# Kernel optimization log

Measured on AMD Instinct MI355X. Metric: run time of the kernel, lower is better.

The kernel has to match this reference:

```python
import jax, jax.numpy as jnp
import numpy as np

B, T, DM, DFE, DH, DRH = 32, 2048, 128, 64, 64, 64
E, NF, NSF, TOPK = 8, 16, 64, 2
LN_EPS = 1e-5


def setup_inputs() -> dict:
    key = jax.random.key(0)
    ks = jax.random.split(key, 18)
    s = 0.05
    # base expert i owns columns [16*i, 16*i+16); scale=2 -> expert e uses base e//2
    expert_idx = jnp.asarray(np.stack([np.arange(NF) + NF * (e // 2) for e in range(E)]), dtype=jnp.int32)  # [E,NF]
    stage_idx = jnp.arange(NSF, dtype=jnp.int32)  # stage uses all 64 columns
    return {
        'hidden': jax.random.normal(ks[0], (B, T, DM), jnp.float32),
        'feat': jax.random.normal(ks[1], (B, T, NSF), jnp.float32),
        'ln_g': jnp.ones((DM,), jnp.float32),
        'ln_b': jnp.zeros((DM,), jnp.float32),
        'Wp': jax.random.normal(ks[2], (NSF, DFE), jnp.float32) * s,
        'bp': jnp.zeros((DFE,), jnp.float32),
        'Wr1': jax.random.normal(ks[3], (DM + DFE, DRH), jnp.float32) * s,
        'br1': jnp.zeros((DRH,), jnp.float32),
        'Wr2': jax.random.normal(ks[4], (DRH, E), jnp.float32) * s,
        'br2': jnp.zeros((E,), jnp.float32),
        'Wf': jax.random.normal(ks[5], (E, NF, DFE), jnp.float32) * s,
        'bf': jnp.zeros((E, DFE), jnp.float32),
        'We1h': jax.random.normal(ks[6], (E, DM, DH), jnp.float32) * s,
        'We1f': jax.random.normal(ks[7], (E, DFE, DH), jnp.float32) * s,
        'be1': jnp.zeros((E, DH), jnp.float32),
        'We2': jax.random.normal(ks[8], (E, DH, DM), jnp.float32) * s,
        'be2': jnp.zeros((E, DM), jnp.float32),
        'alpha': jnp.asarray(1.0, jnp.float32),
        'item_seq_len': jax.random.randint(ks[9], (B,), 1, T + 1),
        'expert_idx': expert_idx,
        'stage_idx': stage_idx,
    }


def _layernorm(x, g, b):
    mu = jnp.mean(x, -1, keepdims=True)
    v = jnp.mean(jnp.square(x - mu), -1, keepdims=True)
    return (x - mu) * jax.lax.rsqrt(v + LN_EPS) * g + b


def reference(hidden, feat, ln_g, ln_b, Wp, bp, Wr1, br1, Wr2, br2,
              Wf, bf, We1h, We1f, be1, We2, be2, alpha,
              item_seq_len, expert_idx, stage_idx):
    h = _layernorm(hidden, ln_g, ln_b)                         # [B,T,DM]  pre_ln
    femb = feat[..., stage_idx] @ Wp + bp                      # [B,T,DFE] stage feature projection
    # --- token router: MLP -> softmax(temp=1) -> top-k renormalized gates ---
    rin = jnp.concatenate([h, femb], -1)                       # [B,T,DM+DFE]
    logits = jax.nn.relu(rin @ Wr1 + br1) @ Wr2 + br2          # [B,T,E]
    probs = jax.nn.softmax(logits, axis=-1)
    topv, topi = jax.lax.top_k(probs, TOPK)                    # [B,T,K]
    topv = topv / jnp.sum(topv, -1, keepdims=True)
    gates = jnp.sum(jax.nn.one_hot(topi, E, dtype=probs.dtype) * topv[..., None], axis=-2)  # [B,T,E]
    valid = jnp.arange(T)[None, :] < item_seq_len[:, None]     # [B,T]
    gates = gates * valid[..., None].astype(gates.dtype)
    # --- experts: per-expert feature gather + 2-layer GELU MLP (hidden + feat inputs) ---
    ef = feat[:, :, expert_idx]                                # [B,T,E,NF] gather
    x = jnp.einsum('btef,efd->bted', ef, Wf) + bf              # [B,T,E,DFE]
    h1 = jax.nn.gelu(jnp.einsum('btd,edo->bteo', h, We1h)
                     + jnp.einsum('bted,edo->bteo', x, We1f) + be1, approximate=False)
    eo = jnp.einsum('bteo,eod->bted', h1, We2) + be2           # [B,T,E,DM]
    moe = jnp.einsum('bte,bted->btd', gates, eo)               # weighted combine
    next_hidden = hidden + alpha * moe                         # residual, alpha_scale=1, dropout=0
    return next_hidden, gates, probs
```

## Files before the change

kernel.cpp:

```cpp
#include <hip/hip_runtime.h>
#include <hip/hip_bf16.h>


typedef unsigned short u16;
typedef __attribute__((ext_vector_type(8))) short bfrag;
typedef __attribute__((ext_vector_type(8))) u16 u16x8;
typedef __attribute__((ext_vector_type(4))) float facc;
typedef __attribute__((ext_vector_type(4))) float f32x4;

#define NTOK 65536
#define CAP 65536

#define OFF_CNT   ((size_t)0)
#define OFF_LTOK  ((size_t)512)
#define OFF_SMAPG (OFF_LTOK + (size_t)8*CAP*4)
#define OFF_HWS   (OFF_SMAPG + (size_t)NTOK*8)
#define OFF_EOTOK (OFF_HWS + (size_t)NTOK*128*2)
#define OFF_W1T   (OFF_EOTOK + (size_t)NTOK*2*128*2)
#define OFF_W2T   (OFF_W1T + 163840)
#define OFF_B1P   (OFF_W2T + 131072)
#define OFF_WPR   (OFF_B1P + 2048)
#define OFF_BR1P  (OFF_WPR + 16384)

__device__ __forceinline__ u16 f2bf(float f) {
  union { __hip_bfloat16 h; u16 u; } cv;
  cv.h = __float2bfloat16(f);
  return cv.u;
}
__device__ __forceinline__ float bf2f(u16 u) {
  return __uint_as_float(((unsigned)u) << 16);
}

__global__ __launch_bounds__(256)
void k0_pre(const float* __restrict__ Wp, const float* __restrict__ bp,
            const float* __restrict__ Wr1, const float* __restrict__ br1,
            const float* __restrict__ Wf, const float* __restrict__ bfv,
            const float* __restrict__ We1h, const float* __restrict__ We1f,
            const float* __restrict__ be1, const float* __restrict__ We2,
            float* __restrict__ Wpr, float* __restrict__ br1p,
            u16* __restrict__ w1t, u16* __restrict__ w2t, float* __restrict__ b1p)
{
  int j = blockIdx.x * 256 + threadIdx.x;
  if (j < 4096) {
    int i = j >> 6, o = j & 63;
    float s = 0.f;
    for (int k = 0; k < 64; ++k) s += Wp[i*64+k] * Wr1[(128+k)*64 + o];
    Wpr[i*64+o] = s;
  } else if (j < 4160) {
    int o = j - 4096;
    float s = br1[o];
    for (int k = 0; k < 64; ++k) s += bp[k] * Wr1[(128+k)*64 + o];
    br1p[o] = s;
  } else if (j < 4160 + 81920) {
    int idx = j - 4160;
    int e = idx / 10240; int rem = idx % 10240;
    int jj = rem / 160; int k = rem % 160;
    float v = 0.f;
    if (k < 128) v = We1h[(e*128 + k)*64 + jj];
    else if (k < 144) {
      int i = k - 128; float s = 0.f;
      for (int d = 0; d < 64; ++d) s += Wf[(e*16+i)*64 + d] * We1f[(e*64+d)*64 + jj];
      v = s;
    }
    w1t[(size_t)(e*64 + jj)*160 + k] = f2bf(v);
  } else if (j < 4160 + 81920 + 65536) {
    int idx = j - 4160 - 81920;
    int e = idx / 8192; int rem = idx % 8192;
    int d = rem / 64; int k = rem & 63;
    w2t[(size_t)(e*128 + d)*64 + k] = f2bf(We2[(e*64 + k)*128 + d]);
  } else if (j < 4160 + 81920 + 65536 + 512) {
    int idx = j - 4160 - 81920 - 65536;
    int e = idx >> 6, o = idx & 63;
    float s = be1[e*64 + o];
    for (int d = 0; d < 64; ++d) s += bfv[e*64 + d] * We1f[(e*64+d)*64 + o];
    b1p[e*64 + o] = s;
  }
}

__global__ __launch_bounds__(256, 4)
void k1_router(const float* __restrict__ hidden, const float* __restrict__ feat,
               const float* __restrict__ ln_g, const float* __restrict__ ln_b,
               const float* __restrict__ Wr1, const float* __restrict__ Wr2,
               const float* __restrict__ br2, const int* __restrict__ seqlen,
               const int* __restrict__ sidx_g,
               const float* __restrict__ Wpr, const float* __restrict__ br1p,
               float* __restrict__ outG, float* __restrict__ outP,
               u16* __restrict__ hws, int* __restrict__ cnt,
               int* __restrict__ listTok, float* __restrict__ smapG)
{
  __shared__ float At[64*64];
  __shared__ float Wc[64*64];
  __shared__ float sW2[512];
  __shared__ float sb1[64], sg[128], sb[128], sbr2[8];
  __shared__ int ssidx[64];
  __shared__ int lcnt[8], lbase[8];
  __shared__ int ltok[8][64];
  __shared__ float tg[64][2];

  int tid = threadIdx.x;

  f32x4 wpf[4];
  #pragma unroll
  for (int u = 0; u < 4; ++u) wpf[u] = ((const f32x4*)Wr1)[u*256 + tid];

  for (int i = tid; i < 512; i += 256) sW2[i] = Wr2[i];
  if (tid < 128) sg[tid] = ln_g[tid]; else sb[tid-128] = ln_b[tid-128];
  if (tid < 64) { sb1[tid] = br1p[tid]; ssidx[tid] = sidx_g[tid]; }
  if (tid >= 64 && tid < 72) sbr2[tid-64] = br2[tid-64];
  if (tid >= 72 && tid < 80) lcnt[tid-72] = 0;
  __syncthreads();

  int tok = tid >> 2, q = tid & 3;
  int t = blockIdx.x * 64 + tok;

  f32x4 x[8];
  #pragma unroll
  for (int i = 0; i < 8; ++i) x[i] = *(const f32x4*)(hidden + (size_t)t*128 + q*32 + i*4);
  float s = 0.f;
  #pragma unroll
  for (int i = 0; i < 8; ++i) { s += x[i][0] + x[i][1]; s += x[i][2] + x[i][3]; }
  s += __shfl_xor(s, 1, 64); s += __shfl_xor(s, 2, 64);
  float mu = s * (1.f/128.f);
  float v = 0.f;
  #pragma unroll
  for (int i = 0; i < 8; ++i) {
    #pragma unroll
    for (int j = 0; j < 4; ++j) { float d = x[i][j] - mu; v = fmaf(d, d, v); }
  }
  v += __shfl_xor(v, 1, 64); v += __shfl_xor(v, 2, 64);
  float rs = rsqrtf(v * (1.f/128.f) + 1e-5f);
  #pragma unroll
  for (int i = 0; i < 8; ++i) {
    #pragma unroll
    for (int j = 0; j < 4; ++j) {
      int c = q*32 + i*4 + j;
      x[i][j] = (x[i][j] - mu) * rs * sg[c] + sb[c];
    }
  }
  #pragma unroll
  for (int m = 0; m < 4; ++m) {
    u16x8 o;
    #pragma unroll
    for (int j = 0; j < 4; ++j) { o[j] = f2bf(x[2*m][j]); o[4+j] = f2bf(x[2*m+1][j]); }
    *(u16x8*)(hws + (size_t)t*128 + q*32 + m*8) = o;
  }
  float fv[16];
  #pragma unroll
  for (int i = 0; i < 16; ++i) fv[i] = feat[(size_t)t*64 + ssidx[q*16 + i]];

  float acc[4][4];
  #pragma unroll
  for (int i = 0; i < 4; ++i)
    #pragma unroll
    for (int p = 0; p < 4; ++p) acc[i][p] = 0.f;

  int tb = tid >> 4;
  int ob = (tid & 15) * 4;

  #pragma unroll 1
  for (int c = 0; c < 3; ++c) {
    if (c < 2) {
      if ((c == 0) ? (q < 2) : (q >= 2)) {
        int kbase = (c == 0) ? q*32 : (q-2)*32;
        #pragma unroll
        for (int i = 0; i < 8; ++i)
          #pragma unroll
          for (int j = 0; j < 4; ++j) {
            int kr = kbase + i*4 + j;
            int slot = ((tok >> 2) ^ (kr & 15) ^ (kr >> 4)) & 15;
            *(float*)((char*)At + (kr << 8) + (slot << 4) + ((tok & 3) << 2)) = x[i][j];
          }
      }
    } else {
      #pragma unroll
      for (int i = 0; i < 16; ++i) {
        int kr = q*16 + i;
        int slot = ((tok >> 2) ^ (kr & 15) ^ (kr >> 4)) & 15;
        *(float*)((char*)At + (kr << 8) + (slot << 4) + ((tok & 3) << 2)) = fv[i];
      }
    }
    #pragma unroll
    for (int u = 0; u < 4; ++u) ((f32x4*)Wc)[u*256 + tid] = wpf[u];
    __syncthreads();
    if (c < 2) {
      const f32x4* nsrc = (c == 0) ? (const f32x4*)(Wr1 + 4096) : (const f32x4*)Wpr;
      #pragma unroll
      for (int u = 0; u < 4; ++u) wpf[u] = nsrc[u*256 + tid];
    }
    #pragma unroll 4
    for (int k = 0; k < 64; ++k) {
      int slot = (tb ^ (k & 15) ^ (k >> 4)) & 15;
      f32x4 a4 = *(const f32x4*)((const char*)At + (k << 8) + (slot << 4));
      f32x4 b4 = *(const f32x4*)(Wc + k*64 + ob);
      #pragma unroll
      for (int i = 0; i < 4; ++i)
        #pragma unroll
        for (int p = 0; p < 4; ++p)
          acc[i][p] = fmaf(a4[i], b4[p], acc[i][p]);
    }
    __syncthreads();
  }

  float w2r[4][8];
  #pragma unroll
  for (int p = 0; p < 4; ++p)
    #pragma unroll
    for (int e = 0; e < 8; ++e) w2r[p][e] = sW2[(ob + p)*8 + e];
  float b1r[4];
  #pragma unroll
  for (int p = 0; p < 4; ++p) b1r[p] = sb1[ob + p];

  int j16 = tid & 15;
  #pragma unroll 1
  for (int ti = 0; ti < 4; ++ti) {
    float lo[8];
    #pragma unroll
    for (int e = 0; e < 8; ++e) lo[e] = 0.f;
    #pragma unroll
    for (int p = 0; p < 4; ++p) {
      float z = fmaxf(acc[ti][p] + b1r[p], 0.f);
      #pragma unroll
      for (int e = 0; e < 8; ++e) lo[e] = fmaf(z, w2r[p][e], lo[e]);
    }
    #pragma unroll
    for (int m = 1; m < 16; m <<= 1) {
      #pragma unroll
      for (int e = 0; e < 8; ++e) lo[e] += __shfl_xor(lo[e], m, 64);
    }
    #pragma unroll
    for (int e = 0; e < 8; ++e) lo[e] += sbr2[e];

    int tloc = tb*4 + ti;
    int tt = blockIdx.x*64 + tloc;
    float mx = lo[0];
    #pragma unroll
    for (int e = 1; e < 8; ++e) mx = fmaxf(mx, lo[e]);
    float ex[8]; float ss = 0.f;
    #pragma unroll
    for (int e = 0; e < 8; ++e) { ex[e] = __expf(lo[e] - mx); ss += ex[e]; }
    float inv = 1.f / ss;
    float p[8];
    #pragma unroll
    for (int e = 0; e < 8; ++e) p[e] = ex[e] * inv;
    float p1 = p[0]; int i1 = 0;
    #pragma unroll
    for (int e = 1; e < 8; ++e) { bool tk2 = p[e] > p1; p1 = tk2 ? p[e] : p1; i1 = tk2 ? e : i1; }
    float p2 = -1.f; int i2 = 0;
    #pragma unroll
    for (int e = 0; e < 8; ++e) { bool tk2 = (e != i1) && (p[e] > p2); p2 = tk2 ? p[e] : p2; i2 = tk2 ? e : i2; }
    bool valid = (tt & 2047) < seqlen[tt >> 11];
    float gden = 1.f / (p1 + p2);
    float g1 = p1 * gden, g2 = p2 * gden;
    float pv = p[0];
    #pragma unroll
    for (int e = 1; e < 8; ++e) pv = (j16 == e) ? p[e] : pv;
    if (j16 < 8) outP[(size_t)tt*8 + j16] = pv;
    float gv = (j16 == i1) ? g1 : ((j16 == i2) ? g2 : 0.f);
    if (!valid) gv = 0.f;
    if (j16 < 8) outG[(size_t)tt*8 + j16] = gv;
    if (j16 == 0) {
      if (valid) {
        int lp = atomicAdd(&lcnt[i1], 1); ltok[i1][lp] = (tt << 1);
        lp = atomicAdd(&lcnt[i2], 1);     ltok[i2][lp] = (tt << 1) | 1;
        tg[tloc][0] = g1; tg[tloc][1] = g2;
      } else {
        tg[tloc][0] = 0.f; tg[tloc][1] = 0.f;
      }
    }
  }

  __syncthreads();
  if (tid < 8) lbase[tid] = atomicAdd(&cnt[tid], lcnt[tid]);
  __syncthreads();
  #pragma unroll 1
  for (int e = 0; e < 8; ++e) {
    int ncnt = lcnt[e];
    if (tid < ncnt) listTok[(size_t)e*CAP + lbase[e] + tid] = ltok[e][tid];
  }
  if (tid < 64) {
    float2 g; g.x = tg[tid][0]; g.y = tg[tid][1];
    ((float2*)smapG)[blockIdx.x*64 + tid] = g;
  }
}

__global__ __launch_bounds__(256)
void k2_experts(const float* __restrict__ feat, const u16* __restrict__ hws,
                const u16* __restrict__ w1t, const u16* __restrict__ w2t,
                const float* __restrict__ b1p, const float* __restrict__ be2,
                const int* __restrict__ eidx_g, const int* __restrict__ cnt,
                const int* __restrict__ listTok, u16* __restrict__ eoTok)
{
  __shared__ u16 Xs[64*168];
  __shared__ u16 H1s[64*88];
  __shared__ float b1s[64], be2s[128];
  __shared__ int sent[64];
  __shared__ int seidx[16];
  __shared__ int snr;

  int b = blockIdx.x, tid = threadIdx.x;
  int e = -1, row0 = 0, n = 0, accb = 0;
  #pragma unroll
  for (int i = 0; i < 8; ++i) {
    int ci = cnt[i]; int ns = (ci + 63) >> 6;
    if (e < 0 && b < accb + ns) { e = i; row0 = (b - accb) << 6; n = ci; }
    accb += ns;
  }
  if (e < 0) return;
  int nr = n - row0; if (nr > 64) nr = 64;
  if (tid == 0) snr = nr;

  if (tid < 64) {
    int ent = (tid < nr) ? listTok[(size_t)e*CAP + row0 + tid] : 0;
    sent[tid] = ent;
    b1s[tid] = b1p[e*64 + tid];
  } else if (tid < 192) {
    be2s[tid - 64] = be2[e*128 + tid - 64];
  } else if (tid < 208) {
    seidx[tid-192] = eidx_g[e*16 + tid - 192];
  }
  __syncthreads();

  for (int c2 = tid; c2 < 1024; c2 += 256) {
    int r = c2 >> 4, p = c2 & 15;
    u16x8 vv = *(const u16x8*)(hws + (size_t)(sent[r] >> 1)*128 + p*8);
    *(u16x8*)((char*)Xs + r*336 + p*16) = vv;
  }
  if (tid < 128) {
    int r = tid >> 1, hf = tid & 1;
    int tk = sent[r] >> 1;
    u16x8 ov;
    #pragma unroll
    for (int p = 0; p < 8; ++p) ov[p] = f2bf(feat[(size_t)tk*64 + seidx[hf*8 + p]]);
    *(u16x8*)((char*)Xs + r*336 + 256 + hf*16) = ov;
    u16x8 zv = {0,0,0,0,0,0,0,0};
    *(u16x8*)((char*)Xs + r*336 + 288 + hf*16) = zv;
  }
  __syncthreads();

  int w = tid >> 6, lane = tid & 63;
  int la = lane & 15, lg = lane >> 4;
  const u16* w1e = w1t + (size_t)e*64*160;
  const u16* w2e = w2t + (size_t)e*128*64;

  facc acc[4];
  #pragma unroll
  for (int ni = 0; ni < 4; ++ni) { facc z = {0.f,0.f,0.f,0.f}; acc[ni] = z; }
  #pragma unroll
  for (int kc = 0; kc < 5; ++kc) {
    int r = w*16 + la;
    bfrag af = *(const bfrag*)((const char*)Xs + r*336 + kc*64 + lg*16);
    #pragma unroll
    for (int ni = 0; ni < 4; ++ni) {
      bfrag bf2 = *(const bfrag*)(w1e + (size_t)(ni*16 + la)*160 + kc*32 + lg*8);
      acc[ni] = __builtin_amdgcn_mfma_f32_16x16x32_bf16(af, bf2, acc[ni], 0, 0, 0);
    }
  }
  #pragma unroll
  for (int ni = 0; ni < 4; ++ni)
    #pragma unroll
    for (int rg = 0; rg < 4; ++rg) {
      int r = w*16 + lg*4 + rg;
      int c = ni*16 + la;
      float z = acc[ni][rg] + b1s[c];
      float gl = 0.5f * z * (1.f + erff(z * 0.70710678118f));
      *(u16*)((char*)H1s + r*176 + c*2) = f2bf(gl);
    }
  __syncthreads();

  facc acc2[8];
  #pragma unroll
  for (int ni = 0; ni < 8; ++ni) { facc z = {0.f,0.f,0.f,0.f}; acc2[ni] = z; }
  #pragma unroll
  for (int kc = 0; kc < 2; ++kc) {
    int r = w*16 + la;
    bfrag af = *(const bfrag*)((const char*)H1s + r*176 + kc*64 + lg*16);
    #pragma unroll
    for (int ni = 0; ni < 8; ++ni) {
      bfrag bf2 = *(const bfrag*)(w2e + (size_t)(ni*16 + la)*64 + kc*32 + lg*8);
      acc2[ni] = __builtin_amdgcn_mfma_f32_16x16x32_bf16(af, bf2, acc2[ni], 0, 0, 0);
    }
  }
  #pragma unroll
  for (int ni = 0; ni < 8; ++ni)
    #pragma unroll
    for (int rg = 0; rg < 4; ++rg) {
      int r = w*16 + lg*4 + rg;
      int c = ni*16 + la;
      if (r < snr) {
        float vv = acc2[ni][rg] + be2s[c];
        eoTok[(size_t)sent[r]*128 + c] = f2bf(vv);
      }
    }
}

__global__ __launch_bounds__(256)
void k3_combine(const float* __restrict__ hidden, const float* __restrict__ smapG,
                const u16* __restrict__ eoTok, const float* __restrict__ alphap,
                float* __restrict__ outN)
{
  int tid = threadIdx.x;
  int tok = tid >> 2, q = tid & 3;
  int t = blockIdx.x*64 + tok;
  float2 g = ((const float2*)smapG)[t];
  float a = alphap[0];
  float ag0 = a * g.x, ag1 = a * g.y;
  const f32x4* hp = (const f32x4*)(hidden + (size_t)t*128 + q*32);
  f32x4* op = (f32x4*)(outN + (size_t)t*128 + q*32);
  const u16x8* e0 = (const u16x8*)(eoTok + ((size_t)t*2)*128 + q*32);
  const u16x8* e1 = (const u16x8*)(eoTok + ((size_t)t*2 + 1)*128 + q*32);
  #pragma unroll
  for (int i = 0; i < 4; ++i) {
    f32x4 r0 = hp[2*i], r1 = hp[2*i+1];
    if (g.x != 0.f) {
      u16x8 x0 = e0[i];
      #pragma unroll
      for (int j = 0; j < 4; ++j) { r0[j] = fmaf(ag0, bf2f(x0[j]), r0[j]); r1[j] = fmaf(ag0, bf2f(x0[4+j]), r1[j]); }
    }
    if (g.y != 0.f) {
      u16x8 x1 = e1[i];
      #pragma unroll
      for (int j = 0; j < 4; ++j) { r0[j] = fmaf(ag1, bf2f(x1[j]), r0[j]); r1[j] = fmaf(ag1, bf2f(x1[4+j]), r1[j]); }
    }
    op[2*i] = r0; op[2*i+1] = r1;
  }
}

extern "C" void kernel_launch(void* const* d_in, const int* in_sizes, int n_in,
                              void* d_out, int out_size, void* d_ws, size_t ws_size,
                              hipStream_t stream) {
  const float* hidden = (const float*)d_in[0];
  const float* feat   = (const float*)d_in[1];
  const float* ln_g   = (const float*)d_in[2];
  const float* ln_b   = (const float*)d_in[3];
  const float* Wp     = (const float*)d_in[4];
  const float* bp     = (const float*)d_in[5];
  const float* Wr1    = (const float*)d_in[6];
  const float* br1    = (const float*)d_in[7];
  const float* Wr2    = (const float*)d_in[8];
  const float* br2    = (const float*)d_in[9];
  const float* Wf     = (const float*)d_in[10];
  const float* bfv    = (const float*)d_in[11];
  const float* We1h   = (const float*)d_in[12];
  const float* We1f   = (const float*)d_in[13];
  const float* be1    = (const float*)d_in[14];
  const float* We2    = (const float*)d_in[15];
  const float* be2    = (const float*)d_in[16];
  const float* alpha  = (const float*)d_in[17];
  const int* seqlen   = (const int*)d_in[18];
  const int* eidx     = (const int*)d_in[19];
  const int* sidx     = (const int*)d_in[20];

  char* ws = (char*)d_ws;
  int*   cnt      = (int*)(ws + OFF_CNT);
  int*   listTok  = (int*)(ws + OFF_LTOK);
  float* smapG    = (float*)(ws + OFF_SMAPG);
  u16*   hws      = (u16*)(ws + OFF_HWS);
  u16*   eoTok    = (u16*)(ws + OFF_EOTOK);
  u16*   w1t      = (u16*)(ws + OFF_W1T);
  u16*   w2t      = (u16*)(ws + OFF_W2T);
  float* b1p      = (float*)(ws + OFF_B1P);
  float* Wpr      = (float*)(ws + OFF_WPR);
  float* br1p     = (float*)(ws + OFF_BR1P);

  float* outN = (float*)d_out;
  float* outG = outN + (size_t)NTOK * 128;
  float* outP = outG + (size_t)NTOK * 8;

  hipMemsetAsync(ws + OFF_CNT, 0, 256, stream);
  k0_pre<<<595, 256, 0, stream>>>(Wp, bp, Wr1, br1, Wf, bfv, We1h, We1f, be1, We2,
                                  Wpr, br1p, w1t, w2t, b1p);
  k1_router<<<1024, 256, 0, stream>>>(hidden, feat, ln_g, ln_b, Wr1, Wr2, br2, seqlen,
                                      sidx, Wpr, br1p, outG, outP, hws, cnt,
                                      listTok, smapG);
  k2_experts<<<2056, 256, 0, stream>>>(feat, hws, w1t, w2t, b1p, be2, eidx,
                                       cnt, listTok, eoTok);
  k3_combine<<<1024, 256, 0, stream>>>(hidden, smapG, eoTok, alpha, outN);
}
```

Baseline: 131.6 us.

## Restructure preprocessing, double router tokens per block, add contiguous-index fast paths

The weight-preprocessing kernel now runs as 25 blocks that stage weights in shared memory and do small tiled matmuls, replacing 595 blocks of scalar dot products. It also writes flags recording whether the stage and expert index arrays are contiguous. The router handles 128 tokens per block with 2 threads per token, which halves its grid, reuses each weight tile over twice as many tokens, and aliases shared buffers. When the flags show contiguous indices, the feature gathers in the router and expert kernels use vectorized loads, and the router per-block lists are capped at 128 entries.

```diff
diff --git a/kernel.cpp b/kernel.cpp
--- a/kernel.cpp
+++ b/kernel.cpp
@@ -12,6 +12,7 @@
 #define CAP 65536
 
 #define OFF_CNT   ((size_t)0)
+#define OFF_FLG   ((size_t)64)
 #define OFF_LTOK  ((size_t)512)
 #define OFF_SMAPG (OFF_LTOK + (size_t)8*CAP*4)
 #define OFF_HWS   (OFF_SMAPG + (size_t)NTOK*8)
@@ -32,187 +33,272 @@
 }
 
 __global__ __launch_bounds__(256)
-void k0_pre(const float* __restrict__ Wp, const float* __restrict__ bp,
-            const float* __restrict__ Wr1, const float* __restrict__ br1,
-            const float* __restrict__ Wf, const float* __restrict__ bfv,
-            const float* __restrict__ We1h, const float* __restrict__ We1f,
-            const float* __restrict__ be1, const float* __restrict__ We2,
-            float* __restrict__ Wpr, float* __restrict__ br1p,
-            u16* __restrict__ w1t, u16* __restrict__ w2t, float* __restrict__ b1p)
+void k0a_pre(const float* __restrict__ Wp, const float* __restrict__ bp,
+             const float* __restrict__ Wr1, const float* __restrict__ br1,
+             const float* __restrict__ Wf, const float* __restrict__ bfv,
+             const float* __restrict__ We1h, const float* __restrict__ We1f,
+             const float* __restrict__ be1, const float* __restrict__ We2,
+             const int* __restrict__ eidx_g, const int* __restrict__ sidx_g,
+             float* __restrict__ Wpr, float* __restrict__ br1p,
+             u16* __restrict__ w1t, u16* __restrict__ w2t, float* __restrict__ b1p,
+             int* __restrict__ flags)
 {
-  int j = blockIdx.x * 256 + threadIdx.x;
-  if (j < 4096) {
-    int i = j >> 6, o = j & 63;
-    float s = 0.f;
-    for (int k = 0; k < 64; ++k) s += Wp[i*64+k] * Wr1[(128+k)*64 + o];
-    Wpr[i*64+o] = s;
-  } else if (j < 4160) {
-    int o = j - 4096;
-    float s = br1[o];
-    for (int k = 0; k < 64; ++k) s += bp[k] * Wr1[(128+k)*64 + o];
-    br1p[o] = s;
-  } else if (j < 4160 + 81920) {
-    int idx = j - 4160;
-    int e = idx / 10240; int rem = idx % 10240;
-    int jj = rem / 160; int k = rem % 160;
-    float v = 0.f;
-    if (k < 128) v = We1h[(e*128 + k)*64 + jj];
-    else if (k < 144) {
-      int i = k - 128; float s = 0.f;
-      for (int d = 0; d < 64; ++d) s += Wf[(e*16+i)*64 + d] * We1f[(e*64+d)*64 + jj];
-      v = s;
-    }
-    w1t[(size_t)(e*64 + jj)*160 + k] = f2bf(v);
-  } else if (j < 4160 + 81920 + 65536) {
-    int idx = j - 4160 - 81920;
-    int e = idx / 8192; int rem = idx % 8192;
-    int d = rem / 64; int k = rem & 63;
-    w2t[(size_t)(e*128 + d)*64 + k] = f2bf(We2[(e*64 + k)*128 + d]);
-  } else if (j < 4160 + 81920 + 65536 + 512) {
-    int idx = j - 4160 - 81920 - 65536;
-    int e = idx >> 6, o = idx & 63;
-    float s = be1[e*64 + o];
-    for (int d = 0; d < 64; ++d) s += bfv[e*64 + d] * We1f[(e*64+d)*64 + o];
-    b1p[e*64 + o] = s;
-  }
-}
-
-__global__ __launch_bounds__(256, 4)
+  __shared__ float smA[64*68];
+  __shared__ float smB[128*68];
+  int b = blockIdx.x, tid = threadIdx.x;
+
+  if (b == 0) {
+    for (int idx = tid; idx < 4096; idx += 256) {
+      int r = idx >> 6, c = idx & 63;
+      smA[r*68 + c] = Wp[idx];
+      smB[r*68 + c] = Wr1[128*64 + idx];
+    }
+    if (tid == 0) { int ok = 1; for (int i = 0; i < 64; ++i) ok &= (sidx_g[i] == i); flags[0] = ok; }
+    __syncthreads();
+    int i = tid >> 2, oq = (tid & 3) * 16;
+    f32x4 acc[4];
+    #pragma unroll
+    for (int m = 0; m < 4; ++m) { f32x4 z = {0,0,0,0}; acc[m] = z; }
+    for (int k = 0; k < 64; ++k) {
+      float a = smA[i*68 + k];
+      #pragma unroll
+      for (int m = 0; m < 4; ++m) {
+        f32x4 b4 = *(const f32x4*)(smB + k*68 + oq + m*4);
+        #pragma unroll
+        for (int j = 0; j < 4; ++j) acc[m][j] = fmaf(a, b4[j], acc[m][j]);
+      }
+    }
+    #pragma unroll
+    for (int m = 0; m < 4; ++m) *(f32x4*)(Wpr + i*64 + oq + m*4) = acc[m];
+    if (tid < 64) {
+      float s = br1[tid];
+      for (int k = 0; k < 64; ++k) s = fmaf(bp[k], smB[k*68 + tid], s);
+      br1p[tid] = s;
+    }
+  } else if (b <= 8) {
+    int e = b - 1;
+    for (int idx = tid; idx < 4096; idx += 256) {
+      int r = idx >> 6, c = idx & 63;
+      smB[r*68 + c] = We1f[e*4096 + idx];
+    }
+    for (int idx = tid; idx < 1024; idx += 256) {
+      int r = idx >> 6, c = idx & 63;
+      smA[r*68 + c] = Wf[e*1024 + idx];
+    }
+    if (tid == 0) {
+      int s0 = eidx_g[e*16]; int ok = 1;
+      for (int i = 0; i < 16; ++i) ok &= (eidx_g[e*16 + i] == s0 + i);
+      flags[1 + e] = ok ? s0 : -1;
+    }
+    __syncthreads();
+    int i = tid >> 4, jq = (tid & 15) * 4;
+    f32x4 acc = {0,0,0,0};
+    for (int d = 0; d < 64; ++d) {
+      float a = smA[i*68 + d];
+      f32x4 b4 = *(const f32x4*)(smB + d*68 + jq);
+      #pragma unroll
+      for (int j = 0; j < 4; ++j) acc[j] = fmaf(a, b4[j], acc[j]);
+    }
+    #pragma unroll
+    for (int j = 0; j < 4; ++j) w1t[(size_t)(e*64 + jq + j)*160 + 128 + i] = f2bf(acc[j]);
+    if (tid < 64) {
+      float s = be1[e*64 + tid];
+      for (int d = 0; d < 64; ++d) s = fmaf(bfv[e*64 + d], smB[d*68 + tid], s);
+      b1p[e*64 + tid] = s;
+    }
+    for (int idx = tid; idx < 1024; idx += 256) {
+      int jj = idx >> 4, kk = idx & 15;
+      w1t[(size_t)(e*64 + jj)*160 + 144 + kk] = 0;
+    }
+  } else if (b <= 16) {
+    int e = b - 9;
+    for (int idx = tid; idx < 8192; idx += 256) {
+      int r = idx >> 6, c = idx & 63;
+      smB[r*68 + c] = We1h[(size_t)e*8192 + idx];
+    }
+    __syncthreads();
+    int jj = tid & 63, kb = (tid >> 6) * 32;
+    #pragma unroll
+    for (int m = 0; m < 4; ++m) {
+      u16x8 o;
+      #pragma unroll
+      for (int q = 0; q < 8; ++q) o[q] = f2bf(smB[(kb + m*8 + q)*68 + jj]);
+      *(u16x8*)(w1t + (size_t)(e*64 + jj)*160 + kb + m*8) = o;
+    }
+  } else if (b <= 24) {
+    int e = b - 17;
+    for (int idx = tid; idx < 8192; idx += 256) {
+      int r = idx >> 7, c = idx & 127;
+      smB[r*132 + c] = We2[(size_t)e*8192 + idx];
+    }
+    __syncthreads();
+    int d = tid & 127, kb = (tid >> 7) * 32;
+    #pragma unroll
+    for (int m = 0; m < 4; ++m) {
+      u16x8 o;
+      #pragma unroll
+      for (int q = 0; q < 8; ++q) o[q] = f2bf(smB[(kb + m*8 + q)*132 + d]);
+      *(u16x8*)(w2t + (size_t)(e*128 + d)*64 + kb + m*8) = o;
+    }
+  }
+}
+
+__global__ __launch_bounds__(256, 3)
 void k1_router(const float* __restrict__ hidden, const float* __restrict__ feat,
                const float* __restrict__ ln_g, const float* __restrict__ ln_b,
                const float* __restrict__ Wr1, const float* __restrict__ Wr2,
                const float* __restrict__ br2, const int* __restrict__ seqlen,
                const int* __restrict__ sidx_g,
                const float* __restrict__ Wpr, const float* __restrict__ br1p,
+               const int* __restrict__ flags,
                float* __restrict__ outG, float* __restrict__ outP,
                u16* __restrict__ hws, int* __restrict__ cnt,
                int* __restrict__ listTok, float* __restrict__ smapG)
 {
-  __shared__ float At[64*64];
+  __shared__ __align__(16) char smemAt[64*128*4];
   __shared__ float Wc[64*64];
-  __shared__ float sW2[512];
-  __shared__ float sb1[64], sg[128], sb[128], sbr2[8];
+  __shared__ float sg[128], sb[128], sb1[64], sbr2[8];
   __shared__ int ssidx[64];
   __shared__ int lcnt[8], lbase[8];
-  __shared__ int ltok[8][64];
-  __shared__ float tg[64][2];
+  float* At = (float*)smemAt;
+  int* ltok = (int*)smemAt;
+  float* tgp = (float*)(smemAt + 4096);
 
   int tid = threadIdx.x;
 
   f32x4 wpf[4];
   #pragma unroll
-  for (int u = 0; u < 4; ++u) wpf[u] = ((const f32x4*)Wr1)[u*256 + tid];
-
-  for (int i = tid; i < 512; i += 256) sW2[i] = Wr2[i];
+  for (int u = 0; u < 4; ++u) wpf[u] = ((const f32x4*)Wpr)[u*256 + tid];
+
   if (tid < 128) sg[tid] = ln_g[tid]; else sb[tid-128] = ln_b[tid-128];
   if (tid < 64) { sb1[tid] = br1p[tid]; ssidx[tid] = sidx_g[tid]; }
   if (tid >= 64 && tid < 72) sbr2[tid-64] = br2[tid-64];
   if (tid >= 72 && tid < 80) lcnt[tid-72] = 0;
-  __syncthreads();
-
-  int tok = tid >> 2, q = tid & 3;
-  int t = blockIdx.x * 64 + tok;
-
-  f32x4 x[8];
-  #pragma unroll
-  for (int i = 0; i < 8; ++i) x[i] = *(const f32x4*)(hidden + (size_t)t*128 + q*32 + i*4);
+  int sidok = flags[0];
+
+  int tl = tid >> 1, hq = tid & 1;
+  int t = blockIdx.x * 128 + tl;
+
+  f32x4 x[16];
+  #pragma unroll
+  for (int i = 0; i < 16; ++i) x[i] = *(const f32x4*)(hidden + (size_t)t*128 + hq*64 + i*4);
   float s = 0.f;
   #pragma unroll
-  for (int i = 0; i < 8; ++i) { s += x[i][0] + x[i][1]; s += x[i][2] + x[i][3]; }
-  s += __shfl_xor(s, 1, 64); s += __shfl_xor(s, 2, 64);
+  for (int i = 0; i < 16; ++i) { s += x[i][0] + x[i][1]; s += x[i][2] + x[i][3]; }
+  s += __shfl_xor(s, 1, 64);
   float mu = s * (1.f/128.f);
   float v = 0.f;
   #pragma unroll
-  for (int i = 0; i < 8; ++i) {
+  for (int i = 0; i < 16; ++i) {
     #pragma unroll
     for (int j = 0; j < 4; ++j) { float d = x[i][j] - mu; v = fmaf(d, d, v); }
   }
-  v += __shfl_xor(v, 1, 64); v += __shfl_xor(v, 2, 64);
+  v += __shfl_xor(v, 1, 64);
   float rs = rsqrtf(v * (1.f/128.f) + 1e-5f);
   #pragma unroll
-  for (int i = 0; i < 8; ++i) {
+  for (int i = 0; i < 16; ++i) {
     #pragma unroll
     for (int j = 0; j < 4; ++j) {
-      int c = q*32 + i*4 + j;
+      int c = hq*64 + i*4 + j;
       x[i][j] = (x[i][j] - mu) * rs * sg[c] + sb[c];
     }
   }
   #pragma unroll
-  for (int m = 0; m < 4; ++m) {
+  for (int m = 0; m < 8; ++m) {
     u16x8 o;
     #pragma unroll
     for (int j = 0; j < 4; ++j) { o[j] = f2bf(x[2*m][j]); o[4+j] = f2bf(x[2*m+1][j]); }
-    *(u16x8*)(hws + (size_t)t*128 + q*32 + m*8) = o;
-  }
-  float fv[16];
-  #pragma unroll
-  for (int i = 0; i < 16; ++i) fv[i] = feat[(size_t)t*64 + ssidx[q*16 + i]];
-
-  float acc[4][4];
-  #pragma unroll
-  for (int i = 0; i < 4; ++i)
+    *(u16x8*)(hws + (size_t)t*128 + hq*64 + m*8) = o;
+  }
+  int tb8 = tl >> 3, t7 = (tl & 7) << 2;
+  if (sidok) {
+    #pragma unroll
+    for (int m = 0; m < 8; ++m) {
+      f32x4 fv = *(const f32x4*)(feat + (size_t)t*64 + hq*32 + m*4);
+      #pragma unroll
+      for (int j = 0; j < 4; ++j) {
+        int kr = hq*32 + m*4 + j;
+        *(float*)((char*)At + (kr << 9) + (((tb8 ^ (kr & 15)) & 15) << 5) + t7) = fv[j];
+      }
+    }
+  } else {
+    #pragma unroll
+    for (int i = 0; i < 32; ++i) {
+      int kr = hq*32 + i;
+      float fv = feat[(size_t)t*64 + ssidx[kr]];
+      *(float*)((char*)At + (kr << 9) + (((tb8 ^ (kr & 15)) & 15) << 5) + t7) = fv;
+    }
+  }
+
+  float acc[8][4];
+  #pragma unroll
+  for (int i = 0; i < 8; ++i)
     #pragma unroll
     for (int p = 0; p < 4; ++p) acc[i][p] = 0.f;
 
-  int tb = tid >> 4;
+  int g8 = tid >> 4;
   int ob = (tid & 15) * 4;
 
   #pragma unroll 1
-  for (int c = 0; c < 3; ++c) {
-    if (c < 2) {
-      if ((c == 0) ? (q < 2) : (q >= 2)) {
-        int kbase = (c == 0) ? q*32 : (q-2)*32;
+  for (int ci = 0; ci < 3; ++ci) {
+    if (ci == 1 && hq == 0) {
+      #pragma unroll
+      for (int i = 0; i < 16; ++i)
         #pragma unroll
-        for (int i = 0; i < 8; ++i)
-          #pragma unroll
-          for (int j = 0; j < 4; ++j) {
-            int kr = kbase + i*4 + j;
-            int slot = ((tok >> 2) ^ (kr & 15) ^ (kr >> 4)) & 15;
-            *(float*)((char*)At + (kr << 8) + (slot << 4) + ((tok & 3) << 2)) = x[i][j];
-          }
-      }
-    } else {
-      #pragma unroll
-      for (int i = 0; i < 16; ++i) {
-        int kr = q*16 + i;
-        int slot = ((tok >> 2) ^ (kr & 15) ^ (kr >> 4)) & 15;
-        *(float*)((char*)At + (kr << 8) + (slot << 4) + ((tok & 3) << 2)) = fv[i];
-      }
+        for (int j = 0; j < 4; ++j) {
+          int kr = i*4 + j;
+          *(float*)((char*)At + (kr << 9) + (((tb8 ^ (kr & 15)) & 15) << 5) + t7) = x[i][j];
+        }
+    }
+    if (ci == 2 && hq == 1) {
+      #pragma unroll
+      for (int i = 0; i < 16; ++i)
+        #pragma unroll
+        for (int j = 0; j < 4; ++j) {
+          int kr = i*4 + j;
+          *(float*)((char*)At + (kr << 9) + (((tb8 ^ (kr & 15)) & 15) << 5) + t7) = x[i][j];
+        }
     }
     #pragma unroll
     for (int u = 0; u < 4; ++u) ((f32x4*)Wc)[u*256 + tid] = wpf[u];
     __syncthreads();
-    if (c < 2) {
-      const f32x4* nsrc = (c == 0) ? (const f32x4*)(Wr1 + 4096) : (const f32x4*)Wpr;
+    if (ci < 2) {
+      const f32x4* nsrc = (ci == 0) ? (const f32x4*)Wr1 : (const f32x4*)(Wr1 + 4096);
       #pragma unroll
       for (int u = 0; u < 4; ++u) wpf[u] = nsrc[u*256 + tid];
     }
     #pragma unroll 4
     for (int k = 0; k < 64; ++k) {
-      int slot = (tb ^ (k & 15) ^ (k >> 4)) & 15;
-      f32x4 a4 = *(const f32x4*)((const char*)At + (k << 8) + (slot << 4));
+      int base = (k << 7) + (((g8 ^ (k & 15)) & 15) << 3);
+      f32x4 a0 = *(const f32x4*)(At + base);
+      f32x4 a1 = *(const f32x4*)(At + base + 4);
       f32x4 b4 = *(const f32x4*)(Wc + k*64 + ob);
       #pragma unroll
       for (int i = 0; i < 4; ++i)
         #pragma unroll
-        for (int p = 0; p < 4; ++p)
-          acc[i][p] = fmaf(a4[i], b4[p], acc[i][p]);
+        for (int p = 0; p < 4; ++p) {
+          acc[i][p]   = fmaf(a0[i], b4[p], acc[i][p]);
+          acc[4+i][p] = fmaf(a1[i], b4[p], acc[4+i][p]);
+        }
     }
     __syncthreads();
   }
 
   float w2r[4][8];
   #pragma unroll
-  for (int p = 0; p < 4; ++p)
-    #pragma unroll
-    for (int e = 0; e < 8; ++e) w2r[p][e] = sW2[(ob + p)*8 + e];
+  for (int p = 0; p < 4; ++p) {
+    f32x4 wlo = *(const f32x4*)(Wr2 + (ob + p)*8);
+    f32x4 whi = *(const f32x4*)(Wr2 + (ob + p)*8 + 4);
+    #pragma unroll
+    for (int e = 0; e < 4; ++e) { w2r[p][e] = wlo[e]; w2r[p][4+e] = whi[e]; }
+  }
   float b1r[4];
   #pragma unroll
   for (int p = 0; p < 4; ++p) b1r[p] = sb1[ob + p];
 
   int j16 = tid & 15;
   #pragma unroll 1
-  for (int ti = 0; ti < 4; ++ti) {
+  for (int ti = 0; ti < 8; ++ti) {
     float lo[8];
     #pragma unroll
     for (int e = 0; e < 8; ++e) lo[e] = 0.f;
@@ -230,8 +316,8 @@
     #pragma unroll
     for (int e = 0; e < 8; ++e) lo[e] += sbr2[e];
 
-    int tloc = tb*4 + ti;
-    int tt = blockIdx.x*64 + tloc;
+    int tloc = g8*8 + ti;
+    int tt = blockIdx.x*128 + tloc;
     float mx = lo[0];
     #pragma unroll
     for (int e = 1; e < 8; ++e) mx = fmaxf(mx, lo[e]);
@@ -260,26 +346,26 @@
     if (j16 < 8) outG[(size_t)tt*8 + j16] = gv;
     if (j16 == 0) {
       if (valid) {
-        int lp = atomicAdd(&lcnt[i1], 1); ltok[i1][lp] = (tt << 1);
-        lp = atomicAdd(&lcnt[i2], 1);     ltok[i2][lp] = (tt << 1) | 1;
-        tg[tloc][0] = g1; tg[tloc][1] = g2;
+        int lp = atomicAdd(&lcnt[i1], 1); if (lp < 128) ltok[i1*128 + lp] = (tt << 1);
+        lp = atomicAdd(&lcnt[i2], 1);     if (lp < 128) ltok[i2*128 + lp] = (tt << 1) | 1;
+        tgp[tloc*2] = g1; tgp[tloc*2+1] = g2;
       } else {
-        tg[tloc][0] = 0.f; tg[tloc][1] = 0.f;
+        tgp[tloc*2] = 0.f; tgp[tloc*2+1] = 0.f;
       }
     }
   }
 
   __syncthreads();
-  if (tid < 8) lbase[tid] = atomicAdd(&cnt[tid], lcnt[tid]);
+  if (tid < 8) { int n8 = min(lcnt[tid], 128); lbase[tid] = atomicAdd(&cnt[tid], n8); }
   __syncthreads();
   #pragma unroll 1
   for (int e = 0; e < 8; ++e) {
-    int ncnt = lcnt[e];
-    if (tid < ncnt) listTok[(size_t)e*CAP + lbase[e] + tid] = ltok[e][tid];
-  }
-  if (tid < 64) {
-    float2 g; g.x = tg[tid][0]; g.y = tg[tid][1];
-    ((float2*)smapG)[blockIdx.x*64 + tid] = g;
+    int ncnt = min(lcnt[e], 128);
+    if (tid < ncnt) listTok[(size_t)e*CAP + lbase[e] + tid] = ltok[e*128 + tid];
+  }
+  if (tid < 128) {
+    float2 g; g.x = tgp[tid*2]; g.y = tgp[tid*2+1];
+    ((float2*)smapG)[blockIdx.x*128 + tid] = g;
   }
 }
 
@@ -288,7 +374,8 @@
                 const u16* __restrict__ w1t, const u16* __restrict__ w2t,
                 const float* __restrict__ b1p, const float* __restrict__ be2,
                 const int* __restrict__ eidx_g, const int* __restrict__ cnt,
-                const int* __restrict__ listTok, u16* __restrict__ eoTok)
+                const int* __restrict__ listTok, const int* __restrict__ flags,
+                u16* __restrict__ eoTok)
 {
   __shared__ u16 Xs[64*168];
   __shared__ u16 H1s[64*88];
@@ -308,6 +395,7 @@
   if (e < 0) return;
   int nr = n - row0; if (nr > 64) nr = 64;
   if (tid == 0) snr = nr;
+  int fb = flags[1 + e];
 
   if (tid < 64) {
     int ent = (tid < nr) ? listTok[(size_t)e*CAP + row0 + tid] : 0;
@@ -329,8 +417,15 @@
     int r = tid >> 1, hf = tid & 1;
     int tk = sent[r] >> 1;
     u16x8 ov;
-    #pragma unroll
-    for (int p = 0; p < 8; ++p) ov[p] = f2bf(feat[(size_t)tk*64 + seidx[hf*8 + p]]);
+    if (fb >= 0) {
+      f32x4 v0 = *(const f32x4*)(feat + (size_t)tk*64 + fb + hf*8);
+      f32x4 v1 = *(const f32x4*)(feat + (size_t)tk*64 + fb + hf*8 + 4);
+      #pragma unroll
+      for (int q = 0; q < 4; ++q) { ov[q] = f2bf(v0[q]); ov[4+q] = f2bf(v1[q]); }
+    } else {
+      #pragma unroll
+      for (int q = 0; q < 8; ++q) ov[q] = f2bf(feat[(size_t)tk*64 + seidx[hf*8 + q]]);
+    }
     *(u16x8*)((char*)Xs + r*336 + 256 + hf*16) = ov;
     u16x8 zv = {0,0,0,0,0,0,0,0};
     *(u16x8*)((char*)Xs + r*336 + 288 + hf*16) = zv;
@@ -452,6 +547,7 @@
 
   char* ws = (char*)d_ws;
   int*   cnt      = (int*)(ws + OFF_CNT);
+  int*   flags    = (int*)(ws + OFF_FLG);
   int*   listTok  = (int*)(ws + OFF_LTOK);
   float* smapG    = (float*)(ws + OFF_SMAPG);
   u16*   hws      = (u16*)(ws + OFF_HWS);
@@ -467,12 +563,12 @@
   float* outP = outG + (size_t)NTOK * 8;
 
   hipMemsetAsync(ws + OFF_CNT, 0, 256, stream);
-  k0_pre<<<595, 256, 0, stream>>>(Wp, bp, Wr1, br1, Wf, bfv, We1h, We1f, be1, We2,
-                                  Wpr, br1p, w1t, w2t, b1p);
-  k1_router<<<1024, 256, 0, stream>>>(hidden, feat, ln_g, ln_b, Wr1, Wr2, br2, seqlen,
-                                      sidx, Wpr, br1p, outG, outP, hws, cnt,
-                                      listTok, smapG);
+  k0a_pre<<<25, 256, 0, stream>>>(Wp, bp, Wr1, br1, Wf, bfv, We1h, We1f, be1, We2,
+                                  eidx, sidx, Wpr, br1p, w1t, w2t, b1p, flags);
+  k1_router<<<512, 256, 0, stream>>>(hidden, feat, ln_g, ln_b, Wr1, Wr2, br2, seqlen,
+                                     sidx, Wpr, br1p, flags, outG, outP, hws, cnt,
+                                     listTok, smapG);
   k2_experts<<<2056, 256, 0, stream>>>(feat, hws, w1t, w2t, b1p, be2, eidx,
-                                       cnt, listTok, eoTok);
+                                       cnt, listTok, flags, eoTok);
   k3_combine<<<1024, 256, 0, stream>>>(hidden, smapG, eoTok, alpha, outN);
 }
```

After: 135.0 us. 1.03x slower.
